# Kernel tuning notes

Measured on AMD Instinct MI355X. Metric: run time of the kernel, lower is better.

## Reference

```python
import jax, jax.numpy as jnp
import numpy as np

NUM_HEADS = 16
HEAD_DIM = 64  # hidden_dim 1024 / 16 heads
COH_DIM = 8
MOT_RANK = 4


def _linear(x, W, b):
    # torch nn.Linear: y = x @ W.T + b
    return jnp.einsum('...i,oi->...o', x, W) + b


def setup_inputs() -> dict:
    key = jax.random.key(0)
    ks = jax.random.split(key, 17)
    d, c, m = HEAD_DIM, COH_DIM, MOT_RANK
    s = 1.0 / np.sqrt(d)
    sc = 1.0 / np.sqrt(c)
    sm = 1.0 / np.sqrt(m)
    inp = {
        'x': jax.random.normal(ks[0], (4, 2048, 1024), dtype=jnp.float32),
        'Wi': jax.random.uniform(ks[1], (d, d), jnp.float32, -s, s),
        'bi': jax.random.uniform(ks[2], (d,), jnp.float32, -s, s),
        'Wq': jax.random.uniform(ks[3], (d, d), jnp.float32, -s, s),
        'bq': jax.random.uniform(ks[4], (d,), jnp.float32, -s, s),
        'Wk': jax.random.uniform(ks[5], (d, d), jnp.float32, -s, s),
        'bk': jax.random.uniform(ks[6], (d,), jnp.float32, -s, s),
        'Wv': jax.random.uniform(ks[7], (d, d), jnp.float32, -s, s),
        'bv': jax.random.uniform(ks[8], (d,), jnp.float32, -s, s),
        'Wc': jax.random.uniform(ks[9], (c, d), jnp.float32, -s, s),
        'bc': jax.random.uniform(ks[10], (c,), jnp.float32, -s, s),
        'Wci': jax.random.uniform(ks[11], (d, c), jnp.float32, -sc, sc),
        'bci': jax.random.uniform(ks[12], (d,), jnp.float32, -sc, sc),
        'Wm': jax.random.uniform(ks[13], (m, d), jnp.float32, -s, s),
        'bm': jax.random.uniform(ks[14], (m,), jnp.float32, -s, s),
        'Wmi': jax.random.uniform(ks[15], (d, m), jnp.float32, -sm, sm),
        'bmi': jax.random.uniform(ks[16], (d,), jnp.float32, -sm, sm),
    }
    return inp


def reference(x, Wi, bi, Wq, bq, Wk, bk, Wv, bv, Wc, bc, Wci, bci, Wm, bm, Wmi, bmi):
    B, S, D = x.shape
    H, hd = NUM_HEADS, HEAD_DIM
    # split heads: [B, H, S, hd]
    xh = x.reshape(B, S, H, hd).transpose(0, 2, 1, 3)
    # resolution * load_factor = 1.0 scaling (identity here), then input projection
    h = _linear(xh, Wi, bi)
    q = _linear(h, Wq, bq)
    k = _linear(h, Wk, bk)
    v = _linear(h, Wv, bv)
    # scaled dot-product attention per head
    scores = jnp.einsum('bhqd,bhkd->bhqk', q, k) / jnp.sqrt(jnp.float32(hd))
    attn = jax.nn.softmax(scores, axis=-1)
    out = jnp.einsum('bhqk,bhkd->bhqd', attn, v)
    # cohomology round-trip projection
    out = _linear(_linear(out, Wc, bc), Wci, bci)
    # motive round-trip projection
    out = _linear(_linear(out, Wm, bm), Wmi, bmi)
    # merge heads back to [B, S, D]
    return out.transpose(0, 2, 1, 3).reshape(B, S, D)
```

## Files before the change

### kernel.cpp

```cpp
#include <hip/hip_runtime.h>


#define SEQ 2048
#define DM  1024
#define HD  64

typedef short bf16x8 __attribute__((ext_vector_type(8)));
typedef unsigned short u16x8 __attribute__((ext_vector_type(8)));
typedef float f32x16 __attribute__((ext_vector_type(16)));

#define MFMA32 __builtin_amdgcn_mfma_f32_32x32x16_bf16

#define KG_OFF  12288
#define VG_OFF  (12288 + 8388608)
#define WS_NEED ((size_t)512 + 2ull * (12288 + 2ull * 8388608))

__device__ __forceinline__ unsigned short f2bf(float f) {
    unsigned int v = __float_as_uint(f);
    unsigned int r = v + 0x7FFFu + ((v >> 16) & 1u);
    return (unsigned short)(r >> 16);
}
__device__ __forceinline__ unsigned int pk2r(float a, float b) {
    return __builtin_amdgcn_perm(__float_as_uint(b) + 0x8000u,
                                 __float_as_uint(a) + 0x8000u, 0x07060302u);
}
__device__ __forceinline__ unsigned int pk2t(float a, float b) {
    return __builtin_amdgcn_perm(__float_as_uint(b), __float_as_uint(a), 0x07060302u);
}
__device__ __forceinline__ f32x16 z16() {
    f32x16 v;
    #pragma unroll
    for (int i = 0; i < 16; i++) v[i] = 0.f;
    return v;
}

__device__ __forceinline__ void mm16(const float* __restrict__ wrow,
                                     const float* __restrict__ L, int i0,
                                     float* __restrict__ acc) {
    #pragma unroll
    for (int ii = 0; ii < 16; ii++) acc[ii] = 0.f;
    for (int t = 0; t < 64; t += 4) {
        float4 w4 = *(const float4*)(wrow + t);
        #pragma unroll
        for (int d = 0; d < 4; d++) {
            float wv = (d == 0) ? w4.x : (d == 1) ? w4.y : (d == 2) ? w4.z : w4.w;
            const float* lr = L + (t + d) * 64 + i0;
            float4 a = *(const float4*)lr;
            float4 b = *(const float4*)(lr + 4);
            float4 c = *(const float4*)(lr + 8);
            float4 e = *(const float4*)(lr + 12);
            acc[0] += wv * a.x;  acc[1] += wv * a.y;  acc[2]  += wv * a.z;  acc[3]  += wv * a.w;
            acc[4] += wv * b.x;  acc[5] += wv * b.y;  acc[6]  += wv * b.z;  acc[7]  += wv * b.w;
            acc[8] += wv * c.x;  acc[9] += wv * c.y;  acc[10] += wv * c.z;  acc[11] += wv * c.w;
            acc[12] += wv * e.x; acc[13] += wv * e.y; acc[14] += wv * e.z;  acc[15] += wv * e.w;
        }
    }
}

__global__ __launch_bounds__(256)
void qmt_combine(const float* __restrict__ Wi,  const float* __restrict__ bi,
                 const float* __restrict__ Wq,  const float* __restrict__ bq,
                 const float* __restrict__ Wk,  const float* __restrict__ bk,
                 const float* __restrict__ Wv,  const float* __restrict__ bv,
                 const float* __restrict__ Wc,  const float* __restrict__ bc,
                 const float* __restrict__ Wci, const float* __restrict__ bci,
                 const float* __restrict__ Wm,  const float* __restrict__ bm,
                 const float* __restrict__ Wmi, const float* __restrict__ bmi,
                 float* __restrict__ ws) {
    const int tid = threadIdx.x;
    const int o = tid & 63;
    const int i0 = (tid >> 6) * 16;
    const bool lead = (tid < 64);

    __shared__ float Wi_s[64 * 64];
    __shared__ float Wvi_s[64 * 64];
    __shared__ float M_s[64 * 64];
    __shared__ float bi_s[64], bvi_s[64], c1[64], c2[4];
    __shared__ float U1[32], U2[4 * 64];

    unsigned short* wsu = (unsigned short*)(ws + 128);

    for (int idx = tid; idx < 4096; idx += 256) Wi_s[idx] = Wi[idx];
    if (lead) bi_s[o] = bi[o];
    __syncthreads();

    float acc[16];
    mm16(Wq + o * 64, Wi_s, i0, acc);
    #pragma unroll
    for (int ii = 0; ii < 16; ii++) wsu[o * 64 + i0 + ii] = f2bf(acc[ii] * 0.125f);
    if (lead) {
        float s = bq[o];
        for (int t = 0; t < 64; t++) s += Wq[o * 64 + t] * bi_s[t];
        ws[o] = s * 0.125f;
    }
    mm16(Wk + o * 64, Wi_s, i0, acc);
    #pragma unroll
    for (int ii = 0; ii < 16; ii++) wsu[4096 + o * 64 + i0 + ii] = f2bf(acc[ii]);
    mm16(Wv + o * 64, Wi_s, i0, acc);
    #pragma unroll
    for (int ii = 0; ii < 16; ii++) Wvi_s[o * 64 + i0 + ii] = acc[ii];
    if (lead) {
        float s = bv[o];
        for (int t = 0; t < 64; t++) s += Wv[o * 64 + t] * bi_s[t];
        bvi_s[o] = s;
    }
    if (tid < 32) {
        int a = tid >> 3, c = tid & 7;
        float s = 0.f;
        for (int t = 0; t < 64; t++) s += Wm[a * 64 + t] * Wci[t * 8 + c];
        U1[a * 8 + c] = s;
    }
    __syncthreads();
    if (lead) {
        for (int a = 0; a < 4; a++) {
            float s = 0.f;
            for (int cc = 0; cc < 8; cc++) s += U1[a * 8 + cc] * Wc[cc * 64 + o];
            U2[a * 64 + o] = s;
        }
        float s = bci[o];
        for (int j = 0; j < 8; j++) s += Wci[o * 8 + j] * bc[j];
        c1[o] = s;
    }
    __syncthreads();
    #pragma unroll
    for (int ii = 0; ii < 16; ii++) {
        float s = 0.f;
        for (int a = 0; a < 4; a++) s += Wmi[o * 4 + a] * U2[a * 64 + i0 + ii];
        M_s[o * 64 + i0 + ii] = s;
    }
    if (tid < 4) {
        float s = bm[tid];
        for (int i = 0; i < 64; i++) s += Wm[tid * 64 + i] * c1[i];
        c2[tid] = s;
    }
    __syncthreads();
    mm16(M_s + o * 64, Wvi_s, i0, acc);
    #pragma unroll
    for (int ii = 0; ii < 16; ii++) wsu[8192 + o * 64 + i0 + ii] = f2bf(acc[ii]);
    if (lead) {
        float bvv = 0.f;
        for (int t = 0; t < 64; t++) bvv += M_s[o * 64 + t] * bvi_s[t];
        float cvv = bmi[o];
        for (int a = 0; a < 4; a++) cvv += Wmi[o * 4 + a] * c2[a];
        ws[64 + o] = cvv + bvv;
    }
}

__global__ __launch_bounds__(256)
void qmt_kv(const float* __restrict__ x, float* __restrict__ ws) {
    const int tid = threadIdx.x;
    const int w = tid >> 6;
    const int lane = tid & 63;
    const int ln = lane & 31;
    const int h = lane >> 5;
    const int kt = blockIdx.x;
    const int b = blockIdx.y >> 4;
    const int hh = blockIdx.y & 15;

    const unsigned short* wsu = (const unsigned short*)(ws + 128);
    unsigned short* Kg = (unsigned short*)(ws + 128) + KG_OFF + (size_t)blockIdx.y * (2048 * 64);
    unsigned short* Vg = (unsigned short*)(ws + 128) + VG_OFF + (size_t)blockIdx.y * (64 * 2048);

    const int krl = (w >> 1) * 32 + ln;
    const int dt32 = (w & 1) * 32;

    bf16x8 akf[4], avf[4];
    #pragma unroll
    for (int c = 0; c < 4; c++) {
        int row = dt32 + ln;
        int col = c * 16 + h * 8;
        akf[c] = *(const bf16x8*)(wsu + 4096 + row * 64 + col);
        avf[c] = *(const bf16x8*)(wsu + 8192 + row * 64 + col);
    }
    bf16x8 xf[4];
    const float* xr = x + ((size_t)(b * SEQ + kt * 64 + krl) * DM + hh * HD);
    #pragma unroll
    for (int c = 0; c < 4; c++) {
        const float* p = xr + c * 16 + h * 8;
        float4 f0 = *(const float4*)p;
        float4 f1 = *(const float4*)(p + 4);
        union { bf16x8 v; unsigned int u[4]; } t;
        t.u[0] = pk2t(f0.x, f0.y); t.u[1] = pk2t(f0.z, f0.w);
        t.u[2] = pk2t(f1.x, f1.y); t.u[3] = pk2t(f1.z, f1.w);
        xf[c] = t.v;
    }
    f32x16 kacc = z16(), vacc = z16();
    #pragma unroll
    for (int c = 0; c < 4; c++) kacc = MFMA32(akf[c], xf[c], kacc, 0, 0, 0);
    #pragma unroll
    for (int c = 0; c < 4; c++) vacc = MFMA32(xf[c], avf[c], vacc, 0, 0, 0);
    #pragma unroll
    for (int g = 0; g < 4; g++) {
        uint2 pk_, pv_;
        pk_.x = pk2r(kacc[4 * g + 0], kacc[4 * g + 1]);
        pk_.y = pk2r(kacc[4 * g + 2], kacc[4 * g + 3]);
        *(uint2*)&Kg[(size_t)(kt * 64 + krl) * 64 + dt32 + 8 * g + 4 * h] = pk_;
        pv_.x = pk2r(vacc[4 * g + 0], vacc[4 * g + 1]);
        pv_.y = pk2r(vacc[4 * g + 2], vacc[4 * g + 3]);
        *(uint2*)&Vg[(size_t)(dt32 + ln) * 2048 + kt * 64 + (w >> 1) * 32 + 8 * g + 4 * h] = pv_;
    }
}

__global__ __launch_bounds__(256, 2)
void qmt_attn2(const float* __restrict__ x, const float* __restrict__ wsf,
               float* __restrict__ out) {
    __shared__ __align__(16) unsigned short ps_s[128 * 72];
    __shared__ __align__(16) unsigned short ks_s[2][64 * 72];
    __shared__ __align__(16) unsigned short vt_s[2][64 * 72];
    __shared__ float als_l[128];
    __shared__ float ls_l[128];

    const int tid = threadIdx.x;
    const int w = tid >> 6;
    const int lane = tid & 63;
    const int ln = lane & 31;
    const int h = lane >> 5;
    const int b = blockIdx.y >> 4;
    const int hh = blockIdx.y & 15;
    const int qbase = blockIdx.x * 128;

    const unsigned short* wsu = (const unsigned short*)(wsf + 128);
    const unsigned short* Kg = wsu + KG_OFF + (size_t)blockIdx.y * (2048 * 64);
    const unsigned short* Vg = wsu + VG_OFF + (size_t)blockIdx.y * (64 * 2048);

    const float ec0 = wsf[64 + ln];
    const float ec1 = wsf[96 + ln];

    bf16x8 qf[4];
    {
        bf16x8 xq[4];
        const float* xrow = x + ((size_t)(b * SEQ + qbase + w * 32 + ln) * DM + hh * HD);
        #pragma unroll
        for (int c = 0; c < 4; c++) {
            const float* p = xrow + c * 16 + h * 8;
            float4 f0 = *(const float4*)p;
            float4 f1 = *(const float4*)(p + 4);
            union { bf16x8 v; unsigned int u[4]; } t;
            t.u[0] = pk2t(f0.x, f0.y); t.u[1] = pk2t(f0.z, f0.w);
            t.u[2] = pk2t(f1.x, f1.y); t.u[3] = pk2t(f1.z, f1.w);
            xq[c] = t.v;
        }
        #pragma unroll
        for (int m = 0; m < 2; m++) {
            f32x16 acc;
            #pragma unroll
            for (int g = 0; g < 4; g++) {
                float4 b4 = *(const float4*)&wsf[m * 32 + 8 * g + 4 * h];
                acc[4 * g + 0] = b4.x; acc[4 * g + 1] = b4.y;
                acc[4 * g + 2] = b4.z; acc[4 * g + 3] = b4.w;
            }
            #pragma unroll
            for (int c = 0; c < 4; c++) {
                bf16x8 aq = *(const bf16x8*)(wsu + (m * 32 + ln) * 64 + c * 16 + h * 8);
                acc = MFMA32(aq, xq[c], acc, 0, 0, 0);
            }
            #pragma unroll
            for (int g = 0; g < 4; g++) {
                uint2 pw;
                pw.x = pk2r(acc[4 * g + 0], acc[4 * g + 1]);
                pw.y = pk2r(acc[4 * g + 2], acc[4 * g + 3]);
                *(uint2*)&ps_s[(w * 32 + ln) * 72 + m * 32 + 8 * g + 4 * h] = pw;
            }
        }
        #pragma unroll
        for (int c = 0; c < 4; c++)
            qf[c] = *(const bf16x8*)&ps_s[(w * 32 + ln) * 72 + c * 16 + h * 8];
    }

    f32x16 o0 = z16(), o1 = z16();
    float m_i = -1e30f, l_i = 0.f;

    const int srow = tid >> 3;
    const int scol = (tid & 7) * 8;

    u16x8 ka, kb, va, vb;
    ka = *(const u16x8*)(Kg + (size_t)srow * 64 + scol);
    kb = *(const u16x8*)(Kg + (size_t)(srow + 32) * 64 + scol);
    va = *(const u16x8*)(Vg + (size_t)srow * 2048 + scol);
    vb = *(const u16x8*)(Vg + (size_t)(srow + 32) * 2048 + scol);
    *(u16x8*)&ks_s[0][srow * 72 + scol] = ka;
    *(u16x8*)&ks_s[0][(srow + 32) * 72 + scol] = kb;
    *(u16x8*)&vt_s[0][srow * 72 + scol] = va;
    *(u16x8*)&vt_s[0][(srow + 32) * 72 + scol] = vb;
    __syncthreads();

    for (int kt = 0; kt < SEQ / 64; kt++) {
        const int cur = kt & 1;
        if (kt < SEQ / 64 - 1) {
            const int kn = (kt + 1) * 64;
            ka = *(const u16x8*)(Kg + (size_t)(kn + srow) * 64 + scol);
            kb = *(const u16x8*)(Kg + (size_t)(kn + srow + 32) * 64 + scol);
            va = *(const u16x8*)(Vg + (size_t)srow * 2048 + kn + scol);
            vb = *(const u16x8*)(Vg + (size_t)(srow + 32) * 2048 + kn + scol);
        }

        f32x16 st0 = z16(), st1 = z16();
        #pragma unroll
        for (int c = 0; c < 4; c++) {
            bf16x8 k0 = *(const bf16x8*)&ks_s[cur][ln * 72 + c * 16 + h * 8];
            bf16x8 k1 = *(const bf16x8*)&ks_s[cur][(32 + ln) * 72 + c * 16 + h * 8];
            st0 = MFMA32(k0, qf[c], st0, 0, 0, 0);
            st1 = MFMA32(k1, qf[c], st1, 0, 0, 0);
        }
        float mx = st0[0];
        #pragma unroll
        for (int i = 1; i < 16; i++) mx = fmaxf(mx, st0[i]);
        #pragma unroll
        for (int i = 0; i < 16; i++) mx = fmaxf(mx, st1[i]);
        mx = fmaxf(mx, __shfl_xor(mx, 32));
        const float mn = fmaxf(m_i, mx);
        const float al = __expf(m_i - mn);
        float ss = 0.f;
        #pragma unroll
        for (int i = 0; i < 16; i++) { st0[i] = __expf(st0[i] - mn); ss += st0[i]; }
        #pragma unroll
        for (int i = 0; i < 16; i++) { st1[i] = __expf(st1[i] - mn); ss += st1[i]; }
        ss += __shfl_xor(ss, 32);
        l_i = l_i * al + ss;
        m_i = mn;
        if (lane < 32) als_l[w * 32 + lane] = al;
        #pragma unroll
        for (int g = 0; g < 4; g++) {
            uint2 p0, p1;
            p0.x = pk2r(st0[4 * g + 0], st0[4 * g + 1]);
            p0.y = pk2r(st0[4 * g + 2], st0[4 * g + 3]);
            *(uint2*)&ps_s[(w * 32 + ln) * 72 + 8 * g + 4 * h] = p0;
            p1.x = pk2r(st1[4 * g + 0], st1[4 * g + 1]);
            p1.y = pk2r(st1[4 * g + 2], st1[4 * g + 3]);
            *(uint2*)&ps_s[(w * 32 + ln) * 72 + 32 + 8 * g + 4 * h] = p1;
        }
        #pragma unroll
        for (int g = 0; g < 4; g++) {
            float4 a4 = *(const float4*)&als_l[w * 32 + 8 * g + 4 * h];
            o0[4 * g + 0] *= a4.x; o0[4 * g + 1] *= a4.y;
            o0[4 * g + 2] *= a4.z; o0[4 * g + 3] *= a4.w;
            o1[4 * g + 0] *= a4.x; o1[4 * g + 1] *= a4.y;
            o1[4 * g + 2] *= a4.z; o1[4 * g + 3] *= a4.w;
        }
        #pragma unroll
        for (int c = 0; c < 4; c++) {
            bf16x8 pf = *(const bf16x8*)&ps_s[(w * 32 + ln) * 72 + c * 16 + h * 8];
            bf16x8 v0 = *(const bf16x8*)&vt_s[cur][ln * 72 + c * 16 + h * 8];
            bf16x8 v1 = *(const bf16x8*)&vt_s[cur][(32 + ln) * 72 + c * 16 + h * 8];
            o0 = MFMA32(pf, v0, o0, 0, 0, 0);
            o1 = MFMA32(pf, v1, o1, 0, 0, 0);
        }
        if (kt < SEQ / 64 - 1) {
            *(u16x8*)&ks_s[1 - cur][srow * 72 + scol] = ka;
            *(u16x8*)&ks_s[1 - cur][(srow + 32) * 72 + scol] = kb;
            *(u16x8*)&vt_s[1 - cur][srow * 72 + scol] = va;
            *(u16x8*)&vt_s[1 - cur][(srow + 32) * 72 + scol] = vb;
        }
        __syncthreads();
    }

    if (lane < 32) ls_l[w * 32 + lane] = l_i;
    #pragma unroll
    for (int g = 0; g < 4; g++) {
        float4 l4 = *(const float4*)&ls_l[w * 32 + 8 * g + 4 * h];
        float4 iv = make_float4(1.f / l4.x, 1.f / l4.y, 1.f / l4.z, 1.f / l4.w);
        #pragma unroll
        for (int i = 0; i < 4; i++) {
            float ivv = (i == 0) ? iv.x : (i == 1) ? iv.y : (i == 2) ? iv.z : iv.w;
            int q = qbase + w * 32 + 8 * g + 4 * h + i;
            float* orow = out + ((size_t)(b * SEQ + q) * DM + hh * HD);
            orow[ln] = o0[4 * g + i] * ivv + ec0;
            orow[32 + ln] = o1[4 * g + i] * ivv + ec1;
        }
    }
}

__global__ __launch_bounds__(256, 3)
void qmt_attn_fb(const float* __restrict__ x, const float* __restrict__ wsf,
                 float* __restrict__ out) {
    __shared__ __align__(16) unsigned short ps_s[128 * 72];
    __shared__ __align__(16) unsigned short ks_s[64 * 72];
    __shared__ __align__(16) unsigned short vt_s[64 * 72];
    __shared__ float als_l[128];
    __shared__ float ls_l[128];

    const int tid = threadIdx.x;
    const int w = tid >> 6;
    const int lane = tid & 63;
    const int ln = lane & 31;
    const int h = lane >> 5;
    const int b = blockIdx.y >> 4;
    const int hh = blockIdx.y & 15;
    const int qbase = blockIdx.x * 128;

    const unsigned short* wsu = (const unsigned short*)(wsf + 128);

    bf16x8 akf[4], avf[4];
    #pragma unroll
    for (int c = 0; c < 4; c++) {
        int row = (w & 1) * 32 + ln;
        int col = c * 16 + h * 8;
        akf[c] = *(const bf16x8*)(wsu + 4096 + row * 64 + col);
        avf[c] = *(const bf16x8*)(wsu + 8192 + row * 64 + col);
    }
    const float ec0 = wsf[64 + ln];
    const float ec1 = wsf[96 + ln];

    bf16x8 qf[4];
    {
        bf16x8 xq[4];
        const float* xrow = x + ((size_t)(b * SEQ + qbase + w * 32 + ln) * DM + hh * HD);
        #pragma unroll
        for (int c = 0; c < 4; c++) {
            const float* p = xrow + c * 16 + h * 8;
            float4 f0 = *(const float4*)p;
            float4 f1 = *(const float4*)(p + 4);
            union { bf16x8 v; unsigned int u[4]; } t;
            t.u[0] = pk2t(f0.x, f0.y); t.u[1] = pk2t(f0.z, f0.w);
            t.u[2] = pk2t(f1.x, f1.y); t.u[3] = pk2t(f1.z, f1.w);
            xq[c] = t.v;
        }
        #pragma unroll
        for (int m = 0; m < 2; m++) {
            f32x16 acc;
            #pragma unroll
            for (int g = 0; g < 4; g++) {
                float4 b4 = *(const float4*)&wsf[m * 32 + 8 * g + 4 * h];
                acc[4 * g + 0] = b4.x; acc[4 * g + 1] = b4.y;
                acc[4 * g + 2] = b4.z; acc[4 * g + 3] = b4.w;
            }
            #pragma unroll
            for (int c = 0; c < 4; c++) {
                bf16x8 aq = *(const bf16x8*)(wsu + (m * 32 + ln) * 64 + c * 16 + h * 8);
                acc = MFMA32(aq, xq[c], acc, 0, 0, 0);
            }
            #pragma unroll
            for (int g = 0; g < 4; g++) {
                uint2 pw;
                pw.x = pk2r(acc[4 * g + 0], acc[4 * g + 1]);
                pw.y = pk2r(acc[4 * g + 2], acc[4 * g + 3]);
                *(uint2*)&ps_s[(w * 32 + ln) * 72 + m * 32 + 8 * g + 4 * h] = pw;
            }
        }
        #pragma unroll
        for (int c = 0; c < 4; c++)
            qf[c] = *(const bf16x8*)&ps_s[(w * 32 + ln) * 72 + c * 16 + h * 8];
    }

    f32x16 o0 = z16(), o1 = z16();
    float m_i = -1e30f, l_i = 0.f;

    const int krl = (w >> 1) * 32 + ln;
    const int dt32 = (w & 1) * 32;

    for (int kt = 0; kt < SEQ / 64; kt++) {
        bf16x8 xf[4];
        const float* xr = x + ((size_t)(b * SEQ + kt * 64 + krl) * DM + hh * HD);
        #pragma unroll
        for (int c = 0; c < 4; c++) {
            const float* p = xr + c * 16 + h * 8;
            float4 f0 = *(const float4*)p;
            float4 f1 = *(const float4*)(p + 4);
            union { bf16x8 v; unsigned int u[4]; } t;
            t.u[0] = pk2t(f0.x, f0.y); t.u[1] = pk2t(f0.z, f0.w);
            t.u[2] = pk2t(f1.x, f1.y); t.u[3] = pk2t(f1.z, f1.w);
            xf[c] = t.v;
        }
        f32x16 kacc = z16(), vacc = z16();
        #pragma unroll
        for (int c = 0; c < 4; c++) kacc = MFMA32(akf[c], xf[c], kacc, 0, 0, 0);
        #pragma unroll
        for (int c = 0; c < 4; c++) vacc = MFMA32(xf[c], avf[c], vacc, 0, 0, 0);
        #pragma unroll
        for (int g = 0; g < 4; g++) {
            uint2 pk_, pv_;
            pk_.x = pk2r(kacc[4 * g + 0], kacc[4 * g + 1]);
            pk_.y = pk2r(kacc[4 * g + 2], kacc[4 * g + 3]);
            *(uint2*)&ks_s[krl * 72 + dt32 + 8 * g + 4 * h] = pk_;
            pv_.x = pk2r(vacc[4 * g + 0], vacc[4 * g + 1]);
            pv_.y = pk2r(vacc[4 * g + 2], vacc[4 * g + 3]);
            *(uint2*)&vt_s[(dt32 + ln) * 72 + (w >> 1) * 32 + 8 * g + 4 * h] = pv_;
        }
        __syncthreads();

        f32x16 st0 = z16(), st1 = z16();
        #pragma unroll
        for (int c = 0; c < 4; c++) {
            bf16x8 k0 = *(const bf16x8*)&ks_s[ln * 72 + c * 16 + h * 8];
            bf16x8 k1 = *(const bf16x8*)&ks_s[(32 + ln) * 72 + c * 16 + h * 8];
            st0 = MFMA32(k0, qf[c], st0, 0, 0, 0);
            st1 = MFMA32(k1, qf[c], st1, 0, 0, 0);
        }
        float mx = st0[0];
        #pragma unroll
        for (int i = 1; i < 16; i++) mx = fmaxf(mx, st0[i]);
        #pragma unroll
        for (int i = 0; i < 16; i++) mx = fmaxf(mx, st1[i]);
        mx = fmaxf(mx, __shfl_xor(mx, 32));
        const float mn = fmaxf(m_i, mx);
        const float al = __expf(m_i - mn);
        float ss = 0.f;
        #pragma unroll
        for (int i = 0; i < 16; i++) { st0[i] = __expf(st0[i] - mn); ss += st0[i]; }
        #pragma unroll
        for (int i = 0; i < 16; i++) { st1[i] = __expf(st1[i] - mn); ss += st1[i]; }
        ss += __shfl_xor(ss, 32);
        l_i = l_i * al + ss;
        m_i = mn;
        if (lane < 32) als_l[w * 32 + lane] = al;
        #pragma unroll
        for (int g = 0; g < 4; g++) {
            uint2 p0, p1;
            p0.x = pk2r(st0[4 * g + 0], st0[4 * g + 1]);
            p0.y = pk2r(st0[4 * g + 2], st0[4 * g + 3]);
            *(uint2*)&ps_s[(w * 32 + ln) * 72 + 8 * g + 4 * h] = p0;
            p1.x = pk2r(st1[4 * g + 0], st1[4 * g + 1]);
            p1.y = pk2r(st1[4 * g + 2], st1[4 * g + 3]);
            *(uint2*)&ps_s[(w * 32 + ln) * 72 + 32 + 8 * g + 4 * h] = p1;
        }
        #pragma unroll
        for (int g = 0; g < 4; g++) {
            float4 a4 = *(const float4*)&als_l[w * 32 + 8 * g + 4 * h];
            o0[4 * g + 0] *= a4.x; o0[4 * g + 1] *= a4.y;
            o0[4 * g + 2] *= a4.z; o0[4 * g + 3] *= a4.w;
            o1[4 * g + 0] *= a4.x; o1[4 * g + 1] *= a4.y;
            o1[4 * g + 2] *= a4.z; o1[4 * g + 3] *= a4.w;
        }
        #pragma unroll
        for (int c = 0; c < 4; c++) {
            bf16x8 pf = *(const bf16x8*)&ps_s[(w * 32 + ln) * 72 + c * 16 + h * 8];
            bf16x8 v0 = *(const bf16x8*)&vt_s[ln * 72 + c * 16 + h * 8];
            bf16x8 v1 = *(const bf16x8*)&vt_s[(32 + ln) * 72 + c * 16 + h * 8];
            o0 = MFMA32(pf, v0, o0, 0, 0, 0);
            o1 = MFMA32(pf, v1, o1, 0, 0, 0);
        }
        __syncthreads();
    }

    if (lane < 32) ls_l[w * 32 + lane] = l_i;
    #pragma unroll
    for (int g = 0; g < 4; g++) {
        float4 l4 = *(const float4*)&ls_l[w * 32 + 8 * g + 4 * h];
        float4 iv = make_float4(1.f / l4.x, 1.f / l4.y, 1.f / l4.z, 1.f / l4.w);
        #pragma unroll
        for (int i = 0; i < 4; i++) {
            float ivv = (i == 0) ? iv.x : (i == 1) ? iv.y : (i == 2) ? iv.z : iv.w;
            int q = qbase + w * 32 + 8 * g + 4 * h + i;
            float* orow = out + ((size_t)(b * SEQ + q) * DM + hh * HD);
            orow[ln] = o0[4 * g + i] * ivv + ec0;
            orow[32 + ln] = o1[4 * g + i] * ivv + ec1;
        }
    }
}

extern "C" void kernel_launch(void* const* d_in, const int* in_sizes, int n_in,
                              void* d_out, int out_size, void* d_ws, size_t ws_size,
                              hipStream_t stream) {
    const float* x = (const float*)d_in[0];
    float* wsf = (float*)d_ws;

    qmt_combine<<<1, 256, 0, stream>>>(
        (const float*)d_in[1],  (const float*)d_in[2],
        (const float*)d_in[3],  (const float*)d_in[4],
        (const float*)d_in[5],  (const float*)d_in[6],
        (const float*)d_in[7],  (const float*)d_in[8],
        (const float*)d_in[9],  (const float*)d_in[10],
        (const float*)d_in[11], (const float*)d_in[12],
        (const float*)d_in[13], (const float*)d_in[14],
        (const float*)d_in[15], (const float*)d_in[16],
        wsf);

    if (ws_size >= WS_NEED) {
        dim3 gkv(SEQ / 64, 64);
        qmt_kv<<<gkv, 256, 0, stream>>>(x, wsf);
        dim3 grid(SEQ / 128, 64);
        qmt_attn2<<<grid, 256, 0, stream>>>(x, wsf, (float*)d_out);
    } else {
        dim3 grid(SEQ / 128, 64);
        qmt_attn_fb<<<grid, 256, 0, stream>>>(x, wsf, (float*)d_out);
    }
}
```

Baseline: 264.7 us.

## Use exp2 softmax, single-buffer attention LDS for higher occupancy, batch KV tiles

```diff
diff --git a/kernel.cpp b/kernel.cpp
--- a/kernel.cpp
+++ b/kernel.cpp
@@ -4,12 +4,22 @@
 #define SEQ 2048
 #define DM  1024
 #define HD  64
+#define QS  0.180336880111120429f
 
 typedef short bf16x8 __attribute__((ext_vector_type(8)));
 typedef unsigned short u16x8 __attribute__((ext_vector_type(8)));
 typedef float f32x16 __attribute__((ext_vector_type(16)));
 
 #define MFMA32 __builtin_amdgcn_mfma_f32_32x32x16_bf16
+
+#if defined(__has_builtin)
+#if __has_builtin(__builtin_amdgcn_exp2f)
+#define EXP2(x) __builtin_amdgcn_exp2f(x)
+#endif
+#endif
+#ifndef EXP2
+#define EXP2(x) exp2f(x)
+#endif
 
 #define KG_OFF  12288
 #define VG_OFF  (12288 + 8388608)
@@ -34,9 +44,9 @@
     return v;
 }
 
-__device__ __forceinline__ void mm16(const float* __restrict__ wrow,
-                                     const float* __restrict__ L, int i0,
-                                     float* __restrict__ acc) {
+__device__ __forceinline__ void mm16L(const float* __restrict__ wrow,
+                                      const float* __restrict__ L, int i0,
+                                      float* __restrict__ acc) {
     #pragma unroll
     for (int ii = 0; ii < 16; ii++) acc[ii] = 0.f;
     for (int t = 0; t < 64; t += 4) {
@@ -44,7 +54,7 @@
         #pragma unroll
         for (int d = 0; d < 4; d++) {
             float wv = (d == 0) ? w4.x : (d == 1) ? w4.y : (d == 2) ? w4.z : w4.w;
-            const float* lr = L + (t + d) * 64 + i0;
+            const float* lr = L + (t + d) * 68 + i0;
             float4 a = *(const float4*)lr;
             float4 b = *(const float4*)(lr + 4);
             float4 c = *(const float4*)(lr + 8);
@@ -72,76 +82,97 @@
     const int i0 = (tid >> 6) * 16;
     const bool lead = (tid < 64);
 
-    __shared__ float Wi_s[64 * 64];
-    __shared__ float Wvi_s[64 * 64];
-    __shared__ float M_s[64 * 64];
+    __shared__ float Wi_s[64 * 68];
+    __shared__ float Wq_s[64 * 68];
+    __shared__ float Wk_s[64 * 68];
+    __shared__ float Wv_s[64 * 68];
+    __shared__ float Wvi_s[64 * 68];
+    __shared__ float M_s[64 * 68];
+    __shared__ float Wc_s[512];
+    __shared__ float Wci_s[512];
+    __shared__ float Wm_s[256];
+    __shared__ float Wmi_s[256];
     __shared__ float bi_s[64], bvi_s[64], c1[64], c2[4];
-    __shared__ float U1[32], U2[4 * 64];
+    __shared__ float U1[32], U2[256];
 
     unsigned short* wsu = (unsigned short*)(ws + 128);
 
-    for (int idx = tid; idx < 4096; idx += 256) Wi_s[idx] = Wi[idx];
+    for (int i4 = tid; i4 < 1024; i4 += 256) {
+        int r = i4 >> 4, c = (i4 & 15) * 4;
+        *(float4*)&Wi_s[r * 68 + c] = *(const float4*)(Wi + i4 * 4);
+        *(float4*)&Wq_s[r * 68 + c] = *(const float4*)(Wq + i4 * 4);
+        *(float4*)&Wk_s[r * 68 + c] = *(const float4*)(Wk + i4 * 4);
+        *(float4*)&Wv_s[r * 68 + c] = *(const float4*)(Wv + i4 * 4);
+    }
+    if (tid < 128) {
+        *(float4*)&Wc_s[tid * 4]  = *(const float4*)(Wc + tid * 4);
+        *(float4*)&Wci_s[tid * 4] = *(const float4*)(Wci + tid * 4);
+    } else if (tid < 192) {
+        int t = tid - 128;
+        *(float4*)&Wm_s[t * 4]  = *(const float4*)(Wm + t * 4);
+        *(float4*)&Wmi_s[t * 4] = *(const float4*)(Wmi + t * 4);
+    }
     if (lead) bi_s[o] = bi[o];
     __syncthreads();
 
     float acc[16];
-    mm16(Wq + o * 64, Wi_s, i0, acc);
-    #pragma unroll
-    for (int ii = 0; ii < 16; ii++) wsu[o * 64 + i0 + ii] = f2bf(acc[ii] * 0.125f);
+    mm16L(Wq_s + o * 68, Wi_s, i0, acc);
+    #pragma unroll
+    for (int ii = 0; ii < 16; ii++) wsu[o * 64 + i0 + ii] = f2bf(acc[ii] * QS);
     if (lead) {
         float s = bq[o];
-        for (int t = 0; t < 64; t++) s += Wq[o * 64 + t] * bi_s[t];
-        ws[o] = s * 0.125f;
-    }
-    mm16(Wk + o * 64, Wi_s, i0, acc);
+        for (int t = 0; t < 64; t++) s += Wq_s[o * 68 + t] * bi_s[t];
+        ws[o] = s * QS;
+    }
+    mm16L(Wk_s + o * 68, Wi_s, i0, acc);
     #pragma unroll
     for (int ii = 0; ii < 16; ii++) wsu[4096 + o * 64 + i0 + ii] = f2bf(acc[ii]);
-    mm16(Wv + o * 64, Wi_s, i0, acc);
-    #pragma unroll
-    for (int ii = 0; ii < 16; ii++) Wvi_s[o * 64 + i0 + ii] = acc[ii];
+    mm16L(Wv_s + o * 68, Wi_s, i0, acc);
+    #pragma unroll
+    for (int ii = 0; ii < 16; ii++) Wvi_s[o * 68 + i0 + ii] = acc[ii];
     if (lead) {
         float s = bv[o];
-        for (int t = 0; t < 64; t++) s += Wv[o * 64 + t] * bi_s[t];
+        for (int t = 0; t < 64; t++) s += Wv_s[o * 68 + t] * bi_s[t];
         bvi_s[o] = s;
     }
     if (tid < 32) {
         int a = tid >> 3, c = tid & 7;
         float s = 0.f;
-        for (int t = 0; t < 64; t++) s += Wm[a * 64 + t] * Wci[t * 8 + c];
+        for (int t = 0; t < 64; t++) s += Wm_s[a * 64 + t] * Wci_s[t * 8 + c];
         U1[a * 8 + c] = s;
     }
     __syncthreads();
     if (lead) {
         for (int a = 0; a < 4; a++) {
             float s = 0.f;
-            for (int cc = 0; cc < 8; cc++) s += U1[a * 8 + cc] * Wc[cc * 64 + o];
+            for (int cc = 0; cc < 8; cc++) s += U1[a * 8 + cc] * Wc_s[cc * 64 + o];
             U2[a * 64 + o] = s;
         }
         float s = bci[o];
-        for (int j = 0; j < 8; j++) s += Wci[o * 8 + j] * bc[j];
+        for (int j = 0; j < 8; j++) s += Wci_s[o * 8 + j] * bc[j];
         c1[o] = s;
     }
     __syncthreads();
     #pragma unroll
     for (int ii = 0; ii < 16; ii++) {
         float s = 0.f;
-        for (int a = 0; a < 4; a++) s += Wmi[o * 4 + a] * U2[a * 64 + i0 + ii];
-        M_s[o * 64 + i0 + ii] = s;
+        for (int a = 0; a < 4; a++) s += Wmi_s[o * 4 + a] * U2[a * 64 + i0 + ii];
+        M_s[o * 68 + i0 + ii] = s;
     }
     if (tid < 4) {
         float s = bm[tid];
-        for (int i = 0; i < 64; i++) s += Wm[tid * 64 + i] * c1[i];
+        for (int i = 0; i < 64; i++) s += Wm_s[tid * 64 + i] * c1[i];
         c2[tid] = s;
     }
     __syncthreads();
-    mm16(M_s + o * 64, Wvi_s, i0, acc);
+    mm16L(M_s + o * 68, Wvi_s, i0, acc);
     #pragma unroll
     for (int ii = 0; ii < 16; ii++) wsu[8192 + o * 64 + i0 + ii] = f2bf(acc[ii]);
     if (lead) {
         float bvv = 0.f;
-        for (int t = 0; t < 64; t++) bvv += M_s[o * 64 + t] * bvi_s[t];
+        for (int t = 0; t < 64; t++) bvv += M_s[o * 68 + t] * bvi_s[t];
         float cvv = bmi[o];
-        for (int a = 0; a < 4; a++) cvv += Wmi[o * 4 + a] * c2[a];
+        for (int a = 0; a < 4; a++) cvv += Wmi_s[o * 4 + a] * c2[a];
         ws[64 + o] = cvv + bvv;
     }
 }
@@ -153,7 +184,6 @@
     const int lane = tid & 63;
     const int ln = lane & 31;
     const int h = lane >> 5;
-    const int kt = blockIdx.x;
     const int b = blockIdx.y >> 4;
     const int hh = blockIdx.y & 15;
 
@@ -172,41 +202,44 @@
         akf[c] = *(const bf16x8*)(wsu + 4096 + row * 64 + col);
         avf[c] = *(const bf16x8*)(wsu + 8192 + row * 64 + col);
     }
-    bf16x8 xf[4];
-    const float* xr = x + ((size_t)(b * SEQ + kt * 64 + krl) * DM + hh * HD);
-    #pragma unroll
-    for (int c = 0; c < 4; c++) {
-        const float* p = xr + c * 16 + h * 8;
-        float4 f0 = *(const float4*)p;
-        float4 f1 = *(const float4*)(p + 4);
-        union { bf16x8 v; unsigned int u[4]; } t;
-        t.u[0] = pk2t(f0.x, f0.y); t.u[1] = pk2t(f0.z, f0.w);
-        t.u[2] = pk2t(f1.x, f1.y); t.u[3] = pk2t(f1.z, f1.w);
-        xf[c] = t.v;
-    }
-    f32x16 kacc = z16(), vacc = z16();
-    #pragma unroll
-    for (int c = 0; c < 4; c++) kacc = MFMA32(akf[c], xf[c], kacc, 0, 0, 0);
-    #pragma unroll
-    for (int c = 0; c < 4; c++) vacc = MFMA32(xf[c], avf[c], vacc, 0, 0, 0);
-    #pragma unroll
-    for (int g = 0; g < 4; g++) {
-        uint2 pk_, pv_;
-        pk_.x = pk2r(kacc[4 * g + 0], kacc[4 * g + 1]);
-        pk_.y = pk2r(kacc[4 * g + 2], kacc[4 * g + 3]);
-        *(uint2*)&Kg[(size_t)(kt * 64 + krl) * 64 + dt32 + 8 * g + 4 * h] = pk_;
-        pv_.x = pk2r(vacc[4 * g + 0], vacc[4 * g + 1]);
-        pv_.y = pk2r(vacc[4 * g + 2], vacc[4 * g + 3]);
-        *(uint2*)&Vg[(size_t)(dt32 + ln) * 2048 + kt * 64 + (w >> 1) * 32 + 8 * g + 4 * h] = pv_;
-    }
-}
-
-__global__ __launch_bounds__(256, 2)
+    for (int t = 0; t < 4; t++) {
+        const int kt = blockIdx.x * 4 + t;
+        bf16x8 xf[4];
+        const float* xr = x + ((size_t)(b * SEQ + kt * 64 + krl) * DM + hh * HD);
+        #pragma unroll
+        for (int c = 0; c < 4; c++) {
+            const float* p = xr + c * 16 + h * 8;
+            float4 f0 = *(const float4*)p;
+            float4 f1 = *(const float4*)(p + 4);
+            union { bf16x8 v; unsigned int u[4]; } tt;
+            tt.u[0] = pk2t(f0.x, f0.y); tt.u[1] = pk2t(f0.z, f0.w);
+            tt.u[2] = pk2t(f1.x, f1.y); tt.u[3] = pk2t(f1.z, f1.w);
+            xf[c] = tt.v;
+        }
+        f32x16 kacc = z16(), vacc = z16();
+        #pragma unroll
+        for (int c = 0; c < 4; c++) kacc = MFMA32(akf[c], xf[c], kacc, 0, 0, 0);
+        #pragma unroll
+        for (int c = 0; c < 4; c++) vacc = MFMA32(xf[c], avf[c], vacc, 0, 0, 0);
+        #pragma unroll
+        for (int g = 0; g < 4; g++) {
+            uint2 pk_, pv_;
+            pk_.x = pk2r(kacc[4 * g + 0], kacc[4 * g + 1]);
+            pk_.y = pk2r(kacc[4 * g + 2], kacc[4 * g + 3]);
+            *(uint2*)&Kg[(size_t)(kt * 64 + krl) * 64 + dt32 + 8 * g + 4 * h] = pk_;
+            pv_.x = pk2r(vacc[4 * g + 0], vacc[4 * g + 1]);
+            pv_.y = pk2r(vacc[4 * g + 2], vacc[4 * g + 3]);
+            *(uint2*)&Vg[(size_t)(dt32 + ln) * 2048 + kt * 64 + (w >> 1) * 32 + 8 * g + 4 * h] = pv_;
+        }
+    }
+}
+
+__global__ __launch_bounds__(256, 4)
 void qmt_attn2(const float* __restrict__ x, const float* __restrict__ wsf,
                float* __restrict__ out) {
     __shared__ __align__(16) unsigned short ps_s[128 * 72];
-    __shared__ __align__(16) unsigned short ks_s[2][64 * 72];
-    __shared__ __align__(16) unsigned short vt_s[2][64 * 72];
+    __shared__ __align__(16) unsigned short ks_s[64 * 72];
+    __shared__ __align__(16) unsigned short vt_s[64 * 72];
     __shared__ float als_l[128];
     __shared__ float ls_l[128];
 
@@ -278,15 +311,15 @@
     kb = *(const u16x8*)(Kg + (size_t)(srow + 32) * 64 + scol);
     va = *(const u16x8*)(Vg + (size_t)srow * 2048 + scol);
     vb = *(const u16x8*)(Vg + (size_t)(srow + 32) * 2048 + scol);
-    *(u16x8*)&ks_s[0][srow * 72 + scol] = ka;
-    *(u16x8*)&ks_s[0][(srow + 32) * 72 + scol] = kb;
-    *(u16x8*)&vt_s[0][srow * 72 + scol] = va;
-    *(u16x8*)&vt_s[0][(srow + 32) * 72 + scol] = vb;
+    *(u16x8*)&ks_s[srow * 72 + scol] = ka;
+    *(u16x8*)&ks_s[(srow + 32) * 72 + scol] = kb;
+    *(u16x8*)&vt_s[srow * 72 + scol] = va;
+    *(u16x8*)&vt_s[(srow + 32) * 72 + scol] = vb;
     __syncthreads();
 
     for (int kt = 0; kt < SEQ / 64; kt++) {
-        const int cur = kt & 1;
-        if (kt < SEQ / 64 - 1) {
+        const bool more = (kt < SEQ / 64 - 1);
+        if (more) {
             const int kn = (kt + 1) * 64;
             ka = *(const u16x8*)(Kg + (size_t)(kn + srow) * 64 + scol);
             kb = *(const u16x8*)(Kg + (size_t)(kn + srow + 32) * 64 + scol);
@@ -297,8 +330,8 @@
         f32x16 st0 = z16(), st1 = z16();
         #pragma unroll
         for (int c = 0; c < 4; c++) {
-            bf16x8 k0 = *(const bf16x8*)&ks_s[cur][ln * 72 + c * 16 + h * 8];
-            bf16x8 k1 = *(const bf16x8*)&ks_s[cur][(32 + ln) * 72 + c * 16 + h * 8];
+            bf16x8 k0 = *(const bf16x8*)&ks_s[ln * 72 + c * 16 + h * 8];
+            bf16x8 k1 = *(const bf16x8*)&ks_s[(32 + ln) * 72 + c * 16 + h * 8];
             st0 = MFMA32(k0, qf[c], st0, 0, 0, 0);
             st1 = MFMA32(k1, qf[c], st1, 0, 0, 0);
         }
@@ -309,12 +342,12 @@
         for (int i = 0; i < 16; i++) mx = fmaxf(mx, st1[i]);
         mx = fmaxf(mx, __shfl_xor(mx, 32));
         const float mn = fmaxf(m_i, mx);
-        const float al = __expf(m_i - mn);
+        const float al = EXP2(m_i - mn);
         float ss = 0.f;
         #pragma unroll
-        for (int i = 0; i < 16; i++) { st0[i] = __expf(st0[i] - mn); ss += st0[i]; }
-        #pragma unroll
-        for (int i = 0; i < 16; i++) { st1[i] = __expf(st1[i] - mn); ss += st1[i]; }
+        for (int i = 0; i < 16; i++) { st0[i] = EXP2(st0[i] - mn); ss += st0[i]; }
+        #pragma unroll
+        for (int i = 0; i < 16; i++) { st1[i] = EXP2(st1[i] - mn); ss += st1[i]; }
         ss += __shfl_xor(ss, 32);
         l_i = l_i * al + ss;
         m_i = mn;
@@ -340,16 +373,17 @@
         #pragma unroll
         for (int c = 0; c < 4; c++) {
             bf16x8 pf = *(const bf16x8*)&ps_s[(w * 32 + ln) * 72 + c * 16 + h * 8];
-            bf16x8 v0 = *(const bf16x8*)&vt_s[cur][ln * 72 + c * 16 + h * 8];
-            bf16x8 v1 = *(const bf16x8*)&vt_s[cur][(32 + ln) * 72 + c * 16 + h * 8];
+            bf16x8 v0 = *(const bf16x8*)&vt_s[ln * 72 + c * 16 + h * 8];
+            bf16x8 v1 = *(const bf16x8*)&vt_s[(32 + ln) * 72 + c * 16 + h * 8];
             o0 = MFMA32(pf, v0, o0, 0, 0, 0);
             o1 = MFMA32(pf, v1, o1, 0, 0, 0);
         }
-        if (kt < SEQ / 64 - 1) {
-            *(u16x8*)&ks_s[1 - cur][srow * 72 + scol] = ka;
-            *(u16x8*)&ks_s[1 - cur][(srow + 32) * 72 + scol] = kb;
-            *(u16x8*)&vt_s[1 - cur][srow * 72 + scol] = va;
-            *(u16x8*)&vt_s[1 - cur][(srow + 32) * 72 + scol] = vb;
+        __syncthreads();
+        if (more) {
+            *(u16x8*)&ks_s[srow * 72 + scol] = ka;
+            *(u16x8*)&ks_s[(srow + 32) * 72 + scol] = kb;
+            *(u16x8*)&vt_s[srow * 72 + scol] = va;
+            *(u16x8*)&vt_s[(srow + 32) * 72 + scol] = vb;
         }
         __syncthreads();
     }
@@ -493,12 +527,12 @@
         for (int i = 0; i < 16; i++) mx = fmaxf(mx, st1[i]);
         mx = fmaxf(mx, __shfl_xor(mx, 32));
         const float mn = fmaxf(m_i, mx);
-        const float al = __expf(m_i - mn);
+        const float al = EXP2(m_i - mn);
         float ss = 0.f;
         #pragma unroll
-        for (int i = 0; i < 16; i++) { st0[i] = __expf(st0[i] - mn); ss += st0[i]; }
-        #pragma unroll
-        for (int i = 0; i < 16; i++) { st1[i] = __expf(st1[i] - mn); ss += st1[i]; }
+        for (int i = 0; i < 16; i++) { st0[i] = EXP2(st0[i] - mn); ss += st0[i]; }
+        #pragma unroll
+        for (int i = 0; i < 16; i++) { st1[i] = EXP2(st1[i] - mn); ss += st1[i]; }
         ss += __shfl_xor(ss, 32);
         l_i = l_i * al + ss;
         m_i = mn;
@@ -566,7 +600,7 @@
         wsf);
 
     if (ws_size >= WS_NEED) {
-        dim3 gkv(SEQ / 64, 64);
+        dim3 gkv(SEQ / 256, 64);
         qmt_kv<<<gkv, 256, 0, stream>>>(x, wsf);
         dim3 grid(SEQ / 128, 64);
         qmt_attn2<<<grid, 256, 0, stream>>>(x, wsf, (float*)d_out);
```

Result: faster. 246.0 us (-7.1%).
